# Performance work log

Measured on AMD Instinct MI355X. Metric: run time of the kernel, lower is better.

The kernel has to match this reference:

```python
import jax, jax.numpy as jnp
import numpy as np

DIM, NHEAD, DM, DL = 512, 8, 64, 128
B, N = 8, 4096


def setup_inputs() -> dict:
    key = jax.random.key(0)
    ks = jax.random.split(key, 6)
    x = jax.random.normal(ks[0], (B, N, DIM), jnp.float32)
    std1 = 1.0 / np.sqrt(DL * DIM).astype(np.float32)
    V = jax.random.uniform(ks[1], (DM, DL), jnp.float32, -std1, std1)
    std2 = np.float32(1.0 / np.sqrt(DL))
    W = jax.random.uniform(ks[2], (NHEAD, DL), jnp.float32, -std2, std2)
    std3 = np.float32(1.0 / np.sqrt(NHEAD * DIM * DM))
    WX = jax.random.uniform(ks[3], (NHEAD, DIM, DM), jnp.float32, -std3, std3)
    std4 = np.float32(1.0 / np.sqrt(DM * DL))
    gate_w = jax.random.uniform(ks[4], (DIM, DL), jnp.float32, -std4, std4)
    # number of valid instances per bag, in [N//2, N]
    true_num = jax.random.randint(ks[5], (B,), N // 2, N + 1)
    return {"x": x, "WX": WX, "V": V, "W": W, "gate_w": gate_w, "true_num": true_num}


def reference(x, WX, V, W, gate_w, true_num):
    Bv, Nv, _ = x.shape
    # per-head instance projections: (H, B, N, dm)
    mh = jnp.einsum('bnd,hdm->hbnm', x, WX)
    # gate is computed from x (identical across heads in the original expand) -> compute once
    gate = jax.nn.sigmoid(jnp.einsum('bnd,dl->bnl', x, gate_w))  # (B, N, dl)
    # gated tanh similarity, then contract with per-head attention vector W
    dis = jnp.tanh(jnp.einsum('hbnm,ml->hbnl', mh, V)) * gate[None]  # (H, B, N, dl)
    scores = jnp.einsum('hbnl,hl->hbn', dis, W)  # (H, B, N)
    # mask out padded instances (index >= true_num[b])
    valid = jnp.arange(Nv)[None, :] < true_num[:, None]  # (B, N)
    scores = jnp.where(valid[None], scores, jnp.float32(-1e20))
    soft = jax.nn.softmax(scores, axis=2)  # (H, B, N)
    # attention-weighted pooling per head, then concat heads: (B, H*dm)
    feat = jnp.einsum('hbn,hbnm->bhm', soft, mh).reshape(Bv, -1)
    return feat, soft[0]
```

## Files before the change

kernel.cpp:

```cpp
#include <hip/hip_runtime.h>
#include <hip/hip_bf16.h>

#define DIM   512
#define NHEAD 8
#define DM    64
#define DL    128
#define BBAG  8
#define NINST 4096
#define MTOT  (BBAG*NINST)
#define NCOL  (NHEAD*DM + DL)
#define NCHUNK 16
#define MH_PITCH 520

typedef short   bf16x8 __attribute__((ext_vector_type(8)));
typedef __bf16  bf16v8 __attribute__((ext_vector_type(8)));
typedef float   f32x4  __attribute__((ext_vector_type(4)));
typedef short   s16x4  __attribute__((ext_vector_type(4)));

__device__ __forceinline__ short f2b(float f) {
  __hip_bfloat16 h = __float2bfloat16(f);
  return __builtin_bit_cast(short, h);
}
__device__ __forceinline__ float b2f(short s) {
  __hip_bfloat16 h = __builtin_bit_cast(__hip_bfloat16, s);
  return __bfloat162float(h);
}
__device__ __forceinline__ f32x4 mfma_bf16(bf16x8 a, bf16x8 b, f32x4 c) {
  return __builtin_amdgcn_mfma_f32_16x16x32_bf16(
      __builtin_bit_cast(bf16v8, a), __builtin_bit_cast(bf16v8, b), c, 0, 0, 0);
}
__device__ __forceinline__ float fast_tanh(float x) {
  float t = __expf(2.0f * x);
  return 1.0f - 2.0f * __builtin_amdgcn_rcpf(t + 1.0f);
}
__device__ __forceinline__ float fast_sigmoid(float x) {
  return __builtin_amdgcn_rcpf(1.0f + __expf(-x));
}

__global__ __launch_bounds__(256) void prep_weights(
    const float* __restrict__ WX, const float* __restrict__ V,
    const float* __restrict__ gate_w,
    short* __restrict__ Wt2, short* __restrict__ Vt_f) {
  __shared__ float lds[32 * 129];
  const int bid = blockIdx.x, t = threadIdx.x;

  if (bid < 128) {
    const int h = bid >> 4, ks = bid & 15;
    {
      const int kl = t >> 3, m8 = (t & 7) * 8;
      const float* src = WX + ((size_t)(h * DIM + ks * 32 + kl) * DM + m8);
      #pragma unroll
      for (int j = 0; j < 8; ++j) lds[kl * 129 + m8 + j] = src[j];
    }
    __syncthreads();
    {
      const int m = t >> 2, q = t & 3;
      const int col = h * 64 + m;
      const int q2 = (q + ((col & 15) >> 1)) & 3;
      short* dst = Wt2 + ks * 20480 + col * 32 + q2 * 8;
      #pragma unroll
      for (int j = 0; j < 8; ++j) dst[j] = f2b(lds[(q * 8 + j) * 129 + m]);
    }
  } else if (bid < 144) {
    const int ks = bid - 128;
    #pragma unroll
    for (int rep = 0; rep < 2; ++rep) {
      const int idx = rep * 2048 + t * 8;
      const int kl = idx >> 7, l8 = idx & 127;
      const float* src = gate_w + ((size_t)(ks * 32 + kl) * DL + l8);
      #pragma unroll
      for (int j = 0; j < 8; ++j) lds[kl * 129 + l8 + j] = src[j];
    }
    __syncthreads();
    #pragma unroll
    for (int rep = 0; rep < 2; ++rep) {
      const int piece = rep * 256 + t;
      const int l = piece >> 2, q = piece & 3;
      const int col = 512 + l;
      const int q2 = (q + ((col & 15) >> 1)) & 3;
      short* dst = Wt2 + ks * 20480 + col * 32 + q2 * 8;
      #pragma unroll
      for (int j = 0; j < 8; ++j) dst[j] = f2b(lds[(q * 8 + j) * 129 + l]);
    }
  } else {
    #pragma unroll
    for (int rep = 0; rep < 4; ++rep) {
      const int e = t + rep * 256;
      const int ct = e >> 7, half = (e >> 6) & 1, lane = e & 63;
      const int r = lane & 15, q = lane >> 4;
      short* dst = Vt_f + (size_t)e * 8;
      #pragma unroll
      for (int j = 0; j < 8; ++j) {
        const int m = half * 32 + q * 8 + j;
        dst[j] = f2b(V[(size_t)m * DL + ct * 16 + r]);
      }
    }
  }
}

#define BLOAD(dst, addr) \
  asm volatile("global_load_dwordx4 %0, %1, off" : "=v"(dst) : "v"(addr))

__global__ __launch_bounds__(512) void proj_score_kernel(
    const float* __restrict__ x, const short* __restrict__ Wt2,
    const short* __restrict__ Vt_f, const float* __restrict__ W,
    short* __restrict__ mh, float* __restrict__ scores) {
  __shared__ alignas(16) short lds[41472];
  const int tid = threadIdx.x;
  const int bm0 = blockIdx.x * 64;
  const int lane = tid & 63;
  const int w = tid >> 6;
  const int r = lane & 15;
  const int q = lane >> 4;
  const int swzs = (q + (r >> 1)) & 3;
  char* lda = reinterpret_cast<char*>(lds);
  short* mh_lds = lds;
  short* gate_lds = lds + 64 * MH_PITCH;

  {
    const int arow = tid >> 3, ap = tid & 7;
    const int aslot = ((ap >> 1) + ((arow & 15) >> 1)) & 3;
    const float* asrc = x + ((size_t)(bm0 + arow) << 9) + (ap << 2);
    char* adst = lda + arow * 64 + aslot * 16 + (ap & 1) * 8;
    #pragma unroll
    for (int ks = 0; ks < 16; ++ks) {
      f32x4 v = *reinterpret_cast<const f32x4*>(asrc + ks * 32);
      s16x4 sv; sv.x = f2b(v[0]); sv.y = f2b(v[1]); sv.z = f2b(v[2]); sv.w = f2b(v[3]);
      *reinterpret_cast<s16x4*>(adst + ks * 4096) = sv;
    }
  }
  __syncthreads();

  const short* bbase = Wt2 + (80 * w + r) * 32 + swzs * 8;
  bf16x8 bufs[3][5];
  #pragma unroll
  for (int ct = 0; ct < 5; ++ct) BLOAD(bufs[0][ct], bbase + 0 * 20480 + ct * 512);
  #pragma unroll
  for (int ct = 0; ct < 5; ++ct) BLOAD(bufs[1][ct], bbase + 1 * 20480 + ct * 512);

  const int aoff = r * 64 + swzs * 16;
  bf16x8 afb[2][4];
  #pragma unroll
  for (int rt = 0; rt < 4; ++rt)
    afb[0][rt] = *reinterpret_cast<const bf16x8*>(lda + 0 * 4096 + aoff + rt * 1024);

  f32x4 acc[4][5];
  #pragma unroll
  for (int rt = 0; rt < 4; ++rt)
    #pragma unroll
    for (int ct = 0; ct < 5; ++ct) acc[rt][ct] = f32x4{0.f, 0.f, 0.f, 0.f};

  #pragma unroll
  for (int ks = 0; ks < 16; ++ks) {
    if (ks + 2 < 16) {
      #pragma unroll
      for (int ct = 0; ct < 5; ++ct)
        BLOAD(bufs[(ks + 2) % 3][ct], bbase + (ks + 2) * 20480 + ct * 512);
    }
    if (ks < 14)      asm volatile("s_waitcnt vmcnt(10)" ::: "memory");
    else if (ks < 15) asm volatile("s_waitcnt vmcnt(5)" ::: "memory");
    else              asm volatile("s_waitcnt vmcnt(0)" ::: "memory");
    __builtin_amdgcn_sched_barrier(0);

    if (ks + 1 < 16) {
      #pragma unroll
      for (int rt = 0; rt < 4; ++rt)
        afb[(ks + 1) & 1][rt] = *reinterpret_cast<const bf16x8*>(
            lda + (ks + 1) * 4096 + aoff + rt * 1024);
    }
    #pragma unroll
    for (int ct = 0; ct < 5; ++ct)
      #pragma unroll
      for (int rt = 0; rt < 4; ++rt)
        acc[rt][ct] = mfma_bf16(afb[ks & 1][rt], bufs[ks % 3][ct], acc[rt][ct]);
  }

  __syncthreads();

  #pragma unroll
  for (int rt = 0; rt < 4; ++rt) {
    #pragma unroll
    for (int ct = 0; ct < 5; ++ct) {
      const int colbase = 80 * w + 16 * ct;
      const int grow0 = bm0 + 16 * rt + 4 * q;
      if (colbase < NHEAD * DM) {
        const int col = colbase + r;
        #pragma unroll
        for (int j = 0; j < 4; ++j) {
          const short bv = f2b(acc[rt][ct][j]);
          mh[((size_t)(col >> 6) * MTOT + grow0 + j) * DM + (col & 63)] = bv;
          mh_lds[(16 * rt + 4 * q + j) * MH_PITCH + col] = bv;
        }
      } else {
        const int ltile = 5 * w + ct - 32;
        s16x4 gv;
        gv.x = f2b(fast_sigmoid(acc[rt][ct][0]));
        gv.y = f2b(fast_sigmoid(acc[rt][ct][1]));
        gv.z = f2b(fast_sigmoid(acc[rt][ct][2]));
        gv.w = f2b(fast_sigmoid(acc[rt][ct][3]));
        *reinterpret_cast<s16x4*>(
            gate_lds + ((rt * 8 + ltile) * 64 + lane) * 4) = gv;
      }
    }
  }
  __syncthreads();

  const int h = w;
  float wc[8];
  #pragma unroll
  for (int lt = 0; lt < 8; ++lt) wc[lt] = W[(size_t)h * DL + 16 * lt + r];

  bf16x8 a0[4], a1[4];
  #pragma unroll
  for (int rt = 0; rt < 4; ++rt) {
    const short* ap = mh_lds + (16 * rt + r) * MH_PITCH + h * 64 + q * 8;
    a0[rt] = *reinterpret_cast<const bf16x8*>(ap);
    a1[rt] = *reinterpret_cast<const bf16x8*>(ap + 32);
  }

  float sc[4][4];
  #pragma unroll
  for (int rt = 0; rt < 4; ++rt)
    #pragma unroll
    for (int j = 0; j < 4; ++j) sc[rt][j] = 0.f;

  #pragma unroll
  for (int lt = 0; lt < 8; ++lt) {
    bf16x8 b0 = *reinterpret_cast<const bf16x8*>(Vt_f + (size_t)(lt * 2) * 512 + lane * 8);
    bf16x8 b1 = *reinterpret_cast<const bf16x8*>(Vt_f + (size_t)(lt * 2 + 1) * 512 + lane * 8);
    #pragma unroll
    for (int rt = 0; rt < 4; ++rt) {
      f32x4 t = f32x4{0.f, 0.f, 0.f, 0.f};
      t = mfma_bf16(a0[rt], b0, t);
      t = mfma_bf16(a1[rt], b1, t);
      s16x4 ga = *reinterpret_cast<const s16x4*>(
          gate_lds + ((rt * 8 + lt) * 64 + lane) * 4);
      #pragma unroll
      for (int j = 0; j < 4; ++j) {
        float g = b2f((j == 0) ? ga.x : (j == 1) ? ga.y : (j == 2) ? ga.z : ga.w);
        sc[rt][j] += fast_tanh(t[j]) * g * wc[lt];
      }
    }
  }

  #pragma unroll
  for (int rt = 0; rt < 4; ++rt) {
    #pragma unroll
    for (int j = 0; j < 4; ++j) {
      sc[rt][j] += __shfl_xor(sc[rt][j], 1);
      sc[rt][j] += __shfl_xor(sc[rt][j], 2);
      sc[rt][j] += __shfl_xor(sc[rt][j], 4);
      sc[rt][j] += __shfl_xor(sc[rt][j], 8);
    }
    if (r < 4) {
      float v = (r == 0) ? sc[rt][0] : (r == 1) ? sc[rt][1]
              : (r == 2) ? sc[rt][2] : sc[rt][3];
      scores[(size_t)h * MTOT + bm0 + 16 * rt + 4 * q + r] = v;
    }
  }
}

__global__ __launch_bounds__(256) void softmax_kernel(
    const float* __restrict__ scores, const int* __restrict__ true_num,
    float* __restrict__ soft, float* __restrict__ out_soft) {
  const int h = blockIdx.x >> 3, b = blockIdx.x & 7;
  const int tid = threadIdx.x;
  const int tn = true_num[b];
  const float* s = scores + ((size_t)h * BBAG + b) * NINST;
  __shared__ float red[8];

  float vals[16];
  float mx = -3.0e38f;
  #pragma unroll
  for (int i = 0; i < 16; ++i) {
    int n = tid + i * 256;
    float v = s[n];
    vals[i] = (n < tn) ? v : -3.0e38f;
    mx = fmaxf(mx, vals[i]);
  }
  #pragma unroll
  for (int m = 1; m < 64; m <<= 1) mx = fmaxf(mx, __shfl_xor(mx, m));
  if ((tid & 63) == 0) red[tid >> 6] = mx;
  __syncthreads();
  mx = fmaxf(fmaxf(red[0], red[1]), fmaxf(red[2], red[3]));

  float sum = 0.f;
  #pragma unroll
  for (int i = 0; i < 16; ++i) {
    int n = tid + i * 256;
    float e = (n < tn) ? expf(vals[i] - mx) : 0.0f;
    vals[i] = e;
    sum += e;
  }
  #pragma unroll
  for (int m = 1; m < 64; m <<= 1) sum += __shfl_xor(sum, m);
  if ((tid & 63) == 0) red[4 + (tid >> 6)] = sum;
  __syncthreads();
  sum = red[4] + red[5] + red[6] + red[7];
  float inv = 1.0f / sum;

  float* so = soft + ((size_t)h * BBAG + b) * NINST;
  #pragma unroll
  for (int i = 0; i < 16; ++i) {
    int n = tid + i * 256;
    float v = vals[i] * inv;
    so[n] = v;
    if (h == 0) out_soft[(size_t)b * NINST + n] = v;
  }
}

__global__ __launch_bounds__(256) void pool_partial(
    const short* __restrict__ mh, const float* __restrict__ soft,
    float* __restrict__ part) {
  const int c = blockIdx.x & (NCHUNK - 1);
  const int hb = blockIdx.x / NCHUNK;
  const int h = hb >> 3, b = hb & 7;
  const int tid = threadIdx.x;
  const int m = tid & 63, g = tid >> 6;
  const int n0 = c * (NINST / NCHUNK);
  const float* so = soft + ((size_t)h * BBAG + b) * NINST;
  const short* mp = mh + ((size_t)h * MTOT + (size_t)b * NINST) * DM;
  float acc = 0.f;
  #pragma unroll 4
  for (int n = n0 + g; n < n0 + NINST / NCHUNK; n += 4) {
    acc += so[n] * b2f(mp[(size_t)n * DM + m]);
  }
  __shared__ float red[256];
  red[tid] = acc;
  __syncthreads();
  if (tid < 64) {
    part[(size_t)(hb * NCHUNK + c) * DM + tid] =
        red[tid] + red[tid + 64] + red[tid + 128] + red[tid + 192];
  }
}

__global__ __launch_bounds__(256) void pool_reduce(
    const float* __restrict__ part, float* __restrict__ out_feat) {
  int g = blockIdx.x * blockDim.x + threadIdx.x;
  int hb = g >> 6, m = g & 63;
  int h = hb >> 3, b = hb & 7;
  float s = 0.f;
  #pragma unroll
  for (int c = 0; c < NCHUNK; ++c)
    s += part[(size_t)(hb * NCHUNK + c) * DM + m];
  out_feat[(size_t)b * (NHEAD * DM) + h * DM + m] = s;
}

extern "C" void kernel_launch(void* const* d_in, const int* in_sizes, int n_in,
                              void* d_out, int out_size, void* d_ws, size_t ws_size,
                              hipStream_t stream) {
  (void)in_sizes; (void)n_in; (void)out_size; (void)ws_size;
  const float* x      = (const float*)d_in[0];
  const float* WX     = (const float*)d_in[1];
  const float* V      = (const float*)d_in[2];
  const float* W      = (const float*)d_in[3];
  const float* gate_w = (const float*)d_in[4];
  const int* true_num = (const int*)d_in[5];
  float* out = (float*)d_out;

  char* ws = (char*)d_ws;
  short* Wt2    = (short*)ws;  ws += (size_t)NCOL * DIM * 2;
  short* Vt_f   = (short*)ws;  ws += (size_t)DL * DM * 2;
  short* mh     = (short*)ws;  ws += (size_t)NHEAD * MTOT * DM * 2;
  float* scores = (float*)ws;  ws += (size_t)NHEAD * MTOT * 4;
  float* soft   = (float*)ws;  ws += (size_t)NHEAD * MTOT * 4;
  float* part   = (float*)ws;  ws += (size_t)NHEAD * BBAG * NCHUNK * DM * 4;

  prep_weights<<<dim3(145), dim3(256), 0, stream>>>(WX, V, gate_w, Wt2, Vt_f);
  proj_score_kernel<<<dim3(MTOT / 64), dim3(512), 0, stream>>>(
      x, Wt2, Vt_f, W, mh, scores);
  softmax_kernel<<<dim3(NHEAD * BBAG), dim3(256), 0, stream>>>(
      scores, true_num, soft, out + BBAG * NHEAD * DM);
  pool_partial<<<dim3(NHEAD * BBAG * NCHUNK), dim3(256), 0, stream>>>(mh, soft, part);
  pool_reduce<<<dim3(NHEAD * BBAG * DM / 256), dim3(256), 0, stream>>>(part, out);
}
```

Before: 71.82 us.

## Fuse softmax and pooling into projection kernel without max subtraction

```diff
diff --git a/kernel.cpp b/kernel.cpp
--- a/kernel.cpp
+++ b/kernel.cpp
@@ -8,8 +8,7 @@
 #define BBAG  8
 #define NINST 4096
 #define MTOT  (BBAG*NINST)
-#define NCOL  (NHEAD*DM + DL)
-#define NCHUNK 16
+#define NBLK  (MTOT/64)
 #define MH_PITCH 520
 
 typedef short   bf16x8 __attribute__((ext_vector_type(8)));
@@ -101,13 +100,16 @@
 #define BLOAD(dst, addr) \
   asm volatile("global_load_dwordx4 %0, %1, off" : "=v"(dst) : "v"(addr))
 
-__global__ __launch_bounds__(512) void proj_score_kernel(
+__global__ __launch_bounds__(512) void fused_kernel(
     const float* __restrict__ x, const short* __restrict__ Wt2,
     const short* __restrict__ Vt_f, const float* __restrict__ W,
-    short* __restrict__ mh, float* __restrict__ scores) {
-  __shared__ alignas(16) short lds[41472];
+    const int* __restrict__ true_num,
+    float* __restrict__ part, float* __restrict__ esum,
+    float* __restrict__ e0) {
+  __shared__ alignas(16) short lds[42496];
   const int tid = threadIdx.x;
-  const int bm0 = blockIdx.x * 64;
+  const int blk = blockIdx.x;
+  const int bm0 = blk * 64;
   const int lane = tid & 63;
   const int w = tid >> 6;
   const int r = lane & 15;
@@ -116,6 +118,10 @@
   char* lda = reinterpret_cast<char*>(lds);
   short* mh_lds = lds;
   short* gate_lds = lds + 64 * MH_PITCH;
+  float* e_lds = reinterpret_cast<float*>(lds + 64 * MH_PITCH + 8192);
+
+  const int tn = true_num[blk >> 6];
+  const int nbase = bm0 & (NINST - 1);
 
   {
     const int arow = tid >> 3, ap = tid & 7;
@@ -182,15 +188,11 @@
     #pragma unroll
     for (int ct = 0; ct < 5; ++ct) {
       const int colbase = 80 * w + 16 * ct;
-      const int grow0 = bm0 + 16 * rt + 4 * q;
       if (colbase < NHEAD * DM) {
         const int col = colbase + r;
         #pragma unroll
-        for (int j = 0; j < 4; ++j) {
-          const short bv = f2b(acc[rt][ct][j]);
-          mh[((size_t)(col >> 6) * MTOT + grow0 + j) * DM + (col & 63)] = bv;
-          mh_lds[(16 * rt + 4 * q + j) * MH_PITCH + col] = bv;
-        }
+        for (int j = 0; j < 4; ++j)
+          mh_lds[(16 * rt + 4 * q + j) * MH_PITCH + col] = f2b(acc[rt][ct][j]);
       } else {
         const int ltile = 5 * w + ct - 32;
         s16x4 gv;
@@ -243,6 +245,7 @@
     }
   }
 
+  float epart = 0.f;
   #pragma unroll
   for (int rt = 0; rt < 4; ++rt) {
     #pragma unroll
@@ -253,97 +256,58 @@
       sc[rt][j] += __shfl_xor(sc[rt][j], 8);
     }
     if (r < 4) {
-      float v = (r == 0) ? sc[rt][0] : (r == 1) ? sc[rt][1]
+      const int row = 16 * rt + 4 * q + r;
+      float s = (r == 0) ? sc[rt][0] : (r == 1) ? sc[rt][1]
               : (r == 2) ? sc[rt][2] : sc[rt][3];
-      scores[(size_t)h * MTOT + bm0 + 16 * rt + 4 * q + r] = v;
-    }
-  }
-}
-
-__global__ __launch_bounds__(256) void softmax_kernel(
-    const float* __restrict__ scores, const int* __restrict__ true_num,
-    float* __restrict__ soft, float* __restrict__ out_soft) {
+      float e = (nbase + row < tn) ? __expf(s) : 0.0f;
+      e_lds[h * 64 + row] = e;
+      epart += e;
+    }
+  }
+  #pragma unroll
+  for (int m = 1; m < 64; m <<= 1) epart += __shfl_xor(epart, m);
+  if (lane == 0) esum[(size_t)h * NBLK + blk] = epart;
+
+  __syncthreads();
+
+  {
+    float P = 0.f;
+    const short* mp = mh_lds + h * 64 + lane;
+    const float* ep = e_lds + h * 64;
+    #pragma unroll 8
+    for (int row = 0; row < 64; ++row)
+      P += ep[row] * b2f(mp[row * MH_PITCH]);
+    part[((size_t)h * NBLK + blk) * 64 + lane] = P;
+  }
+  if (w == 0) e0[bm0 + lane] = e_lds[lane];
+}
+
+__global__ __launch_bounds__(256) void finalize_kernel(
+    const float* __restrict__ part, const float* __restrict__ esum,
+    const float* __restrict__ e0,
+    float* __restrict__ out_feat, float* __restrict__ out_soft) {
   const int h = blockIdx.x >> 3, b = blockIdx.x & 7;
   const int tid = threadIdx.x;
-  const int tn = true_num[b];
-  const float* s = scores + ((size_t)h * BBAG + b) * NINST;
-  __shared__ float red[8];
-
-  float vals[16];
-  float mx = -3.0e38f;
-  #pragma unroll
-  for (int i = 0; i < 16; ++i) {
-    int n = tid + i * 256;
-    float v = s[n];
-    vals[i] = (n < tn) ? v : -3.0e38f;
-    mx = fmaxf(mx, vals[i]);
-  }
-  #pragma unroll
-  for (int m = 1; m < 64; m <<= 1) mx = fmaxf(mx, __shfl_xor(mx, m));
-  if ((tid & 63) == 0) red[tid >> 6] = mx;
-  __syncthreads();
-  mx = fmaxf(fmaxf(red[0], red[1]), fmaxf(red[2], red[3]));
-
-  float sum = 0.f;
-  #pragma unroll
-  for (int i = 0; i < 16; ++i) {
-    int n = tid + i * 256;
-    float e = (n < tn) ? expf(vals[i] - mx) : 0.0f;
-    vals[i] = e;
-    sum += e;
-  }
-  #pragma unroll
-  for (int m = 1; m < 64; m <<= 1) sum += __shfl_xor(sum, m);
-  if ((tid & 63) == 0) red[4 + (tid >> 6)] = sum;
-  __syncthreads();
-  sum = red[4] + red[5] + red[6] + red[7];
-  float inv = 1.0f / sum;
-
-  float* so = soft + ((size_t)h * BBAG + b) * NINST;
-  #pragma unroll
-  for (int i = 0; i < 16; ++i) {
-    int n = tid + i * 256;
-    float v = vals[i] * inv;
-    so[n] = v;
-    if (h == 0) out_soft[(size_t)b * NINST + n] = v;
-  }
-}
-
-__global__ __launch_bounds__(256) void pool_partial(
-    const short* __restrict__ mh, const float* __restrict__ soft,
-    float* __restrict__ part) {
-  const int c = blockIdx.x & (NCHUNK - 1);
-  const int hb = blockIdx.x / NCHUNK;
-  const int h = hb >> 3, b = hb & 7;
-  const int tid = threadIdx.x;
-  const int m = tid & 63, g = tid >> 6;
-  const int n0 = c * (NINST / NCHUNK);
-  const float* so = soft + ((size_t)h * BBAG + b) * NINST;
-  const short* mp = mh + ((size_t)h * MTOT + (size_t)b * NINST) * DM;
-  float acc = 0.f;
-  #pragma unroll 4
-  for (int n = n0 + g; n < n0 + NINST / NCHUNK; n += 4) {
-    acc += so[n] * b2f(mp[(size_t)n * DM + m]);
-  }
-  __shared__ float red[256];
-  red[tid] = acc;
-  __syncthreads();
+
+  float Z = 0.f;
+  #pragma unroll 8
+  for (int c = 0; c < 64; ++c) Z += esum[(size_t)h * NBLK + b * 64 + c];
+  const float invZ = 1.0f / Z;
+
   if (tid < 64) {
-    part[(size_t)(hb * NCHUNK + c) * DM + tid] =
-        red[tid] + red[tid + 64] + red[tid + 128] + red[tid + 192];
-  }
-}
-
-__global__ __launch_bounds__(256) void pool_reduce(
-    const float* __restrict__ part, float* __restrict__ out_feat) {
-  int g = blockIdx.x * blockDim.x + threadIdx.x;
-  int hb = g >> 6, m = g & 63;
-  int h = hb >> 3, b = hb & 7;
-  float s = 0.f;
-  #pragma unroll
-  for (int c = 0; c < NCHUNK; ++c)
-    s += part[(size_t)(hb * NCHUNK + c) * DM + m];
-  out_feat[(size_t)b * (NHEAD * DM) + h * DM + m] = s;
+    float s = 0.f;
+    #pragma unroll 8
+    for (int c = 0; c < 64; ++c)
+      s += part[((size_t)h * NBLK + b * 64 + c) * 64 + tid];
+    out_feat[(size_t)b * (NHEAD * DM) + h * DM + tid] = s * invZ;
+  }
+  if (h == 0) {
+    #pragma unroll
+    for (int i = 0; i < 16; ++i) {
+      const int n = tid + i * 256;
+      out_soft[(size_t)b * NINST + n] = e0[(size_t)b * NINST + n] * invZ;
+    }
+  }
 }
 
 extern "C" void kernel_launch(void* const* d_in, const int* in_sizes, int n_in,
@@ -359,18 +323,15 @@
   float* out = (float*)d_out;
 
   char* ws = (char*)d_ws;
-  short* Wt2    = (short*)ws;  ws += (size_t)NCOL * DIM * 2;
-  short* Vt_f   = (short*)ws;  ws += (size_t)DL * DM * 2;
-  short* mh     = (short*)ws;  ws += (size_t)NHEAD * MTOT * DM * 2;
-  float* scores = (float*)ws;  ws += (size_t)NHEAD * MTOT * 4;
-  float* soft   = (float*)ws;  ws += (size_t)NHEAD * MTOT * 4;
-  float* part   = (float*)ws;  ws += (size_t)NHEAD * BBAG * NCHUNK * DM * 4;
+  short* Wt2  = (short*)ws;  ws += (size_t)(NHEAD * DM + DL) * DIM * 2;
+  short* Vt_f = (short*)ws;  ws += (size_t)DL * DM * 2;
+  float* part = (float*)ws;  ws += (size_t)NHEAD * NBLK * 64 * 4;
+  float* esum = (float*)ws;  ws += (size_t)NHEAD * NBLK * 4;
+  float* e0   = (float*)ws;  ws += (size_t)MTOT * 4;
 
   prep_weights<<<dim3(145), dim3(256), 0, stream>>>(WX, V, gate_w, Wt2, Vt_f);
-  proj_score_kernel<<<dim3(MTOT / 64), dim3(512), 0, stream>>>(
-      x, Wt2, Vt_f, W, mh, scores);
-  softmax_kernel<<<dim3(NHEAD * BBAG), dim3(256), 0, stream>>>(
-      scores, true_num, soft, out + BBAG * NHEAD * DM);
-  pool_partial<<<dim3(NHEAD * BBAG * NCHUNK), dim3(256), 0, stream>>>(mh, soft, part);
-  pool_reduce<<<dim3(NHEAD * BBAG * DM / 256), dim3(256), 0, stream>>>(part, out);
-}
+  fused_kernel<<<dim3(NBLK), dim3(512), 0, stream>>>(
+      x, Wt2, Vt_f, W, true_num, part, esum, e0);
+  finalize_kernel<<<dim3(NHEAD * BBAG), dim3(256), 0, stream>>>(
+      part, esum, e0, out, out + BBAG * NHEAD * DM);
+}
```

Measured after the change: 66.08 us. 8.0% less time.
